# Optimization experiments

Hardware: AMD Instinct MI355X
Metric: run time of the kernel (lower is better)

The kernel has to match this reference:

```python
import jax, jax.numpy as jnp
import numpy as np

H = 64       # hidden_size
V = 200000   # vocab_size
B = 1024     # batch (sessions)
N = 50       # unique nodes per session graph
S = 50       # session sequence length


def setup_inputs() -> dict:
    key = jax.random.key(0)
    ks = jax.random.split(key, 24)
    s = 0.05
    lin = lambda k, i, o: jax.random.normal(k, (i, o), jnp.float32) * s  # stored [in,out]
    return {
        "alias_inputs": jax.random.randint(ks[0], (B, S), 0, N),
        "ain": jax.random.uniform(ks[1], (B, N, N), jnp.float32) * 0.1,
        "aou": jax.random.uniform(ks[2], (B, N, N), jnp.float32) * 0.1,
        "items": jax.random.randint(ks[3], (B, N), 0, V),
        "mask": jnp.ones((B, S), jnp.int32),
        "edge_index": jnp.zeros((2, 1), jnp.int32),
        "emb": jax.random.normal(ks[4], (V, H), jnp.float32) * s,
        "ein_w": lin(ks[5], H, H), "ein_b": jnp.zeros((H,), jnp.float32),
        "eou_w": lin(ks[6], H, H), "eou_b": jnp.zeros((H,), jnp.float32),
        "b_iah": jax.random.normal(ks[7], (H,), jnp.float32) * s,
        "b_oah": jax.random.normal(ks[8], (H,), jnp.float32) * s,
        "igate_w": lin(ks[9], 2 * H, 3 * H), "igate_b": jnp.zeros((3 * H,), jnp.float32),
        "hgate_w": lin(ks[10], H, 3 * H), "hgate_b": jnp.zeros((3 * H,), jnp.float32),
        "fc1_w": lin(ks[11], H, H), "fc1_b": jnp.zeros((H,), jnp.float32),
        "fc2_w": lin(ks[12], H, H), "fc2_b": jnp.zeros((H,), jnp.float32),
        "fc3_w": lin(ks[13], H, 1),
    }


def _forward(alias_inputs, ain, aou, items, mask, emb,
             ein_w, ein_b, eou_w, eou_b, b_iah, b_oah,
             igate_w, igate_b, hgate_w, hgate_b,
             fc1_w, fc1_b, fc2_w, fc2_b, fc3_w):
    STEP = 1
    h = emb[items]  # [B,N,H]
    for _ in range(STEP):
        # GRU-style gated graph conv cell
        input_in = jnp.matmul(ain, h @ ein_w + ein_b) + b_iah    # [B,N,H]
        input_out = jnp.matmul(aou, h @ eou_w + eou_b) + b_oah   # [B,N,H]
        inputs = jnp.concatenate([input_in, input_out], axis=-1)  # [B,N,2H]
        gi = inputs @ igate_w + igate_b                          # [B,N,3H]
        gh = h @ hgate_w + hgate_b                               # [B,N,3H]
        i_r, i_i, i_n = jnp.split(gi, 3, axis=-1)
        h_r, h_i, h_n = jnp.split(gh, 3, axis=-1)
        resetgate = jax.nn.sigmoid(i_r + h_r)
        inputgate = jax.nn.sigmoid(i_i + h_i)
        newgate = jnp.tanh(i_n + resetgate * h_n)
        h = newgate + inputgate * (h - newgate)
    # batch_emb: gather node states back to sequence order
    seq = jnp.take_along_axis(h, alias_inputs[..., None], axis=1)  # [B,S,H]
    # attention readout
    last = jnp.sum(mask, axis=1) - 1                               # [B]
    ht = seq[jnp.arange(seq.shape[0]), last]                       # [B,H]
    q1 = (ht @ fc1_w + fc1_b)[:, None, :]                          # [B,1,H]
    q2 = seq @ fc2_w + fc2_b                                       # [B,S,H]
    alpha = jax.nn.sigmoid(q1 + q2) @ fc3_w                        # [B,S,1]
    a = jnp.sum(alpha * seq * mask[..., None].astype(seq.dtype), axis=1)  # [B,H]
    return a @ emb[1:].T                                           # [B,V-1]


def reference(alias_inputs, ain, aou, items, mask, edge_index, emb,
              ein_w, ein_b, eou_w, eou_b, b_iah, b_oah,
              igate_w, igate_b, hgate_w, hgate_b,
              fc1_w, fc1_b, fc2_w, fc2_b, fc3_w):
    del edge_index  # unused in the original forward
    return _forward(alias_inputs, ain, aou, items, mask, emb,
                    ein_w, ein_b, eou_w, eou_b, b_iah, b_oah,
                    igate_w, igate_b, hgate_w, hgate_b,
                    fc1_w, fc1_b, fc2_w, fc2_b, fc3_w)
```

## Files before the change

kernel.cpp:

```cpp
#include <hip/hip_runtime.h>
#include <math.h>

#define H 64
#define N 50
#define S 50
#define B 1024
#define V 200000
#define VO (V - 1)

__global__ __launch_bounds__(64) void k1_embed_lin(
    const int* __restrict__ items, const float* __restrict__ emb,
    const float* __restrict__ ein_w, const float* __restrict__ ein_b,
    const float* __restrict__ eou_w, const float* __restrict__ eou_b,
    float* __restrict__ h0, float* __restrict__ hv_in, float* __restrict__ hv_out)
{
    int bn = blockIdx.x;
    int j = threadIdx.x;
    __shared__ float hrow[H];
    int item = items[bn];
    float h = emb[(size_t)item * H + j];
    hrow[j] = h;
    h0[(size_t)bn * H + j] = h;
    __syncthreads();
    float si = ein_b[j], so = eou_b[j];
    #pragma unroll
    for (int k = 0; k < H; k++) {
        float x = hrow[k];
        si += x * ein_w[k * H + j];
        so += x * eou_w[k * H + j];
    }
    hv_in[(size_t)bn * H + j] = si;
    hv_out[(size_t)bn * H + j] = so;
}

__global__ __launch_bounds__(64) void k2_adj(
    const float* __restrict__ ain, const float* __restrict__ aou,
    const float* __restrict__ hv_in, const float* __restrict__ hv_out,
    const float* __restrict__ b_iah, const float* __restrict__ b_oah,
    float* __restrict__ in_in, float* __restrict__ in_out)
{
    int bn = blockIdx.x;
    int b = bn / N;
    int j = threadIdx.x;
    const float* ar = ain + (size_t)bn * N;
    const float* br = aou + (size_t)bn * N;
    const float* hin = hv_in + (size_t)b * N * H;
    const float* hou = hv_out + (size_t)b * N * H;
    float si = b_iah[j], so = b_oah[j];
    for (int m = 0; m < N; m++) {
        si += ar[m] * hin[m * H + j];
        so += br[m] * hou[m * H + j];
    }
    in_in[(size_t)bn * H + j] = si;
    in_out[(size_t)bn * H + j] = so;
}

__global__ __launch_bounds__(64) void k3_gru(
    const float* __restrict__ in_in, const float* __restrict__ in_out,
    const float* __restrict__ igate_w, const float* __restrict__ igate_b,
    const float* __restrict__ hgate_w, const float* __restrict__ hgate_b,
    float* __restrict__ h0)
{
    int bn = blockIdx.x;
    int j = threadIdx.x;
    __shared__ float inp[2 * H];
    __shared__ float hrow[H];
    inp[j]     = in_in[(size_t)bn * H + j];
    inp[H + j] = in_out[(size_t)bn * H + j];
    hrow[j]    = h0[(size_t)bn * H + j];
    __syncthreads();
    float gr = igate_b[j], gi = igate_b[H + j], gn = igate_b[2 * H + j];
    for (int k = 0; k < 2 * H; k++) {
        float x = inp[k];
        const float* w = igate_w + (size_t)k * 3 * H;
        gr += x * w[j];
        gi += x * w[H + j];
        gn += x * w[2 * H + j];
    }
    float hr = hgate_b[j], hi = hgate_b[H + j], hn = hgate_b[2 * H + j];
    for (int k = 0; k < H; k++) {
        float x = hrow[k];
        const float* w = hgate_w + (size_t)k * 3 * H;
        hr += x * w[j];
        hi += x * w[H + j];
        hn += x * w[2 * H + j];
    }
    float resetg = 1.f / (1.f + expf(-(gr + hr)));
    float inputg = 1.f / (1.f + expf(-(gi + hi)));
    float newg = tanhf(gn + resetg * hn);
    float h = hrow[j];
    h0[(size_t)bn * H + j] = newg + inputg * (h - newg);
}

__global__ __launch_bounds__(64) void k4_attn(
    const int* __restrict__ alias_in, const int* __restrict__ mask,
    const float* __restrict__ h,
    const float* __restrict__ fc1_w, const float* __restrict__ fc1_b,
    const float* __restrict__ fc2_w, const float* __restrict__ fc2_b,
    const float* __restrict__ fc3_w, float* __restrict__ a)
{
    int b = blockIdx.x;
    int j = threadIdx.x;
    __shared__ float seq[S][H];
    __shared__ float q1s[H];
    const float* hb = h + (size_t)b * N * H;
    for (int s = 0; s < S; s++) {
        int node = alias_in[b * S + s];
        seq[s][j] = hb[(size_t)node * H + j];
    }
    int msum = 0;
    for (int s = 0; s < S; s++) msum += mask[b * S + s];
    int last = msum - 1;
    __syncthreads();
    float q1 = fc1_b[j];
    for (int k = 0; k < H; k++) q1 += seq[last][k] * fc1_w[k * H + j];
    q1s[j] = q1;
    __syncthreads();
    float f3 = fc3_w[j];
    float aj = 0.f;
    for (int s = 0; s < S; s++) {
        float q2 = fc2_b[j];
        for (int k = 0; k < H; k++) q2 += seq[s][k] * fc2_w[k * H + j];
        float v = (1.f / (1.f + expf(-(q1s[j] + q2)))) * f3;
        #pragma unroll
        for (int off = 1; off < 64; off <<= 1) v += __shfl_xor(v, off, 64);
        aj += v * seq[s][j] * (float)mask[b * S + s];
    }
    a[b * H + j] = aj;
}

__global__ __launch_bounds__(256) void k5_out(
    const float* __restrict__ a, const float* __restrict__ emb,
    float* __restrict__ out)
{
    __shared__ __align__(16) float As[64][68];
    __shared__ __align__(16) float Es[64][68];
    int tid = threadIdx.x;
    int tx = tid & 15, ty = tid >> 4;
    int v0 = blockIdx.x * 64;
    int b0 = blockIdx.y * 64;

    for (int idx = tid; idx < 64 * 16; idx += 256) {
        int row = idx >> 4, k4 = idx & 15;
        float4 av = *(const float4*)(a + (size_t)(b0 + row) * H + k4 * 4);
        *(float4*)&As[row][k4 * 4] = av;
        int v = v0 + row;
        float4 ev = make_float4(0.f, 0.f, 0.f, 0.f);
        if (v < VO) ev = *(const float4*)(emb + (size_t)(v + 1) * H + k4 * 4);
        *(float4*)&Es[row][k4 * 4] = ev;
    }
    __syncthreads();

    float acc[4][4] = {};
    #pragma unroll 4
    for (int k4 = 0; k4 < 16; k4++) {
        float4 af[4], ef[4];
        #pragma unroll
        for (int i = 0; i < 4; i++)
            af[i] = *(const float4*)&As[ty + 16 * i][k4 * 4];
        #pragma unroll
        for (int jj = 0; jj < 4; jj++)
            ef[jj] = *(const float4*)&Es[tx + 16 * jj][k4 * 4];
        #pragma unroll
        for (int i = 0; i < 4; i++)
            #pragma unroll
            for (int jj = 0; jj < 4; jj++)
                acc[i][jj] += af[i].x * ef[jj].x + af[i].y * ef[jj].y +
                              af[i].z * ef[jj].z + af[i].w * ef[jj].w;
    }

    #pragma unroll
    for (int i = 0; i < 4; i++) {
        int b = b0 + ty + 16 * i;
        #pragma unroll
        for (int jj = 0; jj < 4; jj++) {
            int v = v0 + tx + 16 * jj;
            if (v < VO) out[(size_t)b * VO + v] = acc[i][jj];
        }
    }
}

extern "C" void kernel_launch(void* const* d_in, const int* in_sizes, int n_in,
                              void* d_out, int out_size, void* d_ws, size_t ws_size,
                              hipStream_t stream)
{
    const int*   alias_in = (const int*)d_in[0];
    const float* ain      = (const float*)d_in[1];
    const float* aou      = (const float*)d_in[2];
    const int*   items    = (const int*)d_in[3];
    const int*   mask     = (const int*)d_in[4];
    const float* emb      = (const float*)d_in[6];
    const float* ein_w    = (const float*)d_in[7];
    const float* ein_b    = (const float*)d_in[8];
    const float* eou_w    = (const float*)d_in[9];
    const float* eou_b    = (const float*)d_in[10];
    const float* b_iah    = (const float*)d_in[11];
    const float* b_oah    = (const float*)d_in[12];
    const float* igate_w  = (const float*)d_in[13];
    const float* igate_b  = (const float*)d_in[14];
    const float* hgate_w  = (const float*)d_in[15];
    const float* hgate_b  = (const float*)d_in[16];
    const float* fc1_w    = (const float*)d_in[17];
    const float* fc1_b    = (const float*)d_in[18];
    const float* fc2_w    = (const float*)d_in[19];
    const float* fc2_b    = (const float*)d_in[20];
    const float* fc3_w    = (const float*)d_in[21];

    float* out = (float*)d_out;

    const size_t NH = (size_t)B * N * H;
    float* h0     = out;
    float* hv_in  = h0 + NH;
    float* hv_out = hv_in + NH;
    float* in_in  = hv_out + NH;
    float* in_out = in_in + NH;
    float* a      = (float*)d_ws;

    k1_embed_lin<<<B * N, 64, 0, stream>>>(items, emb, ein_w, ein_b, eou_w, eou_b,
                                           h0, hv_in, hv_out);
    k2_adj<<<B * N, 64, 0, stream>>>(ain, aou, hv_in, hv_out, b_iah, b_oah,
                                     in_in, in_out);
    k3_gru<<<B * N, 64, 0, stream>>>(in_in, in_out, igate_w, igate_b,
                                     hgate_w, hgate_b, h0);
    k4_attn<<<B, 64, 0, stream>>>(alias_in, mask, h0, fc1_w, fc1_b,
                                  fc2_w, fc2_b, fc3_w, a);
    dim3 g5((VO + 63) / 64, B / 64);
    k5_out<<<g5, 256, 0, stream>>>(a, emb, out);
}
```

Measured before the change: 1.562 ms.

## Retile all kernels with 256-thread blocks and register blocking over rows

Every kernel is restructured. The embedding-linear and GRU kernels now process 32 rows per 256-thread block, with each warp computing 8 rows in registers so weight loads are reused. The adjacency kernel stages a whole session's node features in shared memory once per batch. The attention kernel splits the sequence across 4 warps and caches fc2_w in shared memory. The output GEMM grows to 128x128 tiles with 8x8 per-thread accumulators and an unguarded fast store path. The aim is to cut redundant global weight traffic and raise arithmetic intensity, at the cost of higher register pressure.

```diff
diff --git a/kernel.cpp b/kernel.cpp
--- a/kernel.cpp
+++ b/kernel.cpp
@@ -8,142 +8,247 @@
 #define V 200000
 #define VO (V - 1)
 
-__global__ __launch_bounds__(64) void k1_embed_lin(
+__global__ __launch_bounds__(256) void k1_embed_lin(
     const int* __restrict__ items, const float* __restrict__ emb,
     const float* __restrict__ ein_w, const float* __restrict__ ein_b,
     const float* __restrict__ eou_w, const float* __restrict__ eou_b,
     float* __restrict__ h0, float* __restrict__ hv_in, float* __restrict__ hv_out)
 {
-    int bn = blockIdx.x;
-    int j = threadIdx.x;
-    __shared__ float hrow[H];
-    int item = items[bn];
-    float h = emb[(size_t)item * H + j];
-    hrow[j] = h;
-    h0[(size_t)bn * H + j] = h;
-    __syncthreads();
-    float si = ein_b[j], so = eou_b[j];
+    int tid = threadIdx.x;
+    int j = tid & 63, w = tid >> 6;
+    int bn0 = blockIdx.x * 32;
+    __shared__ __align__(16) float hs[32][H];
+
+    for (int idx = tid; idx < 32 * H; idx += 256) {
+        int row = idx >> 6, col = idx & 63;
+        int item = items[bn0 + row];
+        float hv = emb[(size_t)item * H + col];
+        hs[row][col] = hv;
+        h0[(size_t)(bn0 + row) * H + col] = hv;
+    }
+    __syncthreads();
+
+    float accI[8], accO[8];
+    {
+        float bi = ein_b[j], bo = eou_b[j];
+        #pragma unroll
+        for (int r = 0; r < 8; r++) { accI[r] = bi; accO[r] = bo; }
+    }
+    int base = w * 8;
+    #pragma unroll 4
+    for (int k4 = 0; k4 < 16; k4++) {
+        float4 xv[8];
+        #pragma unroll
+        for (int r = 0; r < 8; r++)
+            xv[r] = *(const float4*)&hs[base + r][k4 * 4];
+        #pragma unroll
+        for (int kk = 0; kk < 4; kk++) {
+            int k = k4 * 4 + kk;
+            float wi = ein_w[k * H + j];
+            float wo = eou_w[k * H + j];
+            #pragma unroll
+            for (int r = 0; r < 8; r++) {
+                float x = ((const float*)&xv[r])[kk];
+                accI[r] += x * wi;
+                accO[r] += x * wo;
+            }
+        }
+    }
     #pragma unroll
-    for (int k = 0; k < H; k++) {
-        float x = hrow[k];
-        si += x * ein_w[k * H + j];
-        so += x * eou_w[k * H + j];
-    }
-    hv_in[(size_t)bn * H + j] = si;
-    hv_out[(size_t)bn * H + j] = so;
-}
-
-__global__ __launch_bounds__(64) void k2_adj(
+    for (int r = 0; r < 8; r++) {
+        hv_in [(size_t)(bn0 + base + r) * H + j] = accI[r];
+        hv_out[(size_t)(bn0 + base + r) * H + j] = accO[r];
+    }
+}
+
+__global__ __launch_bounds__(256) void k2_adj(
     const float* __restrict__ ain, const float* __restrict__ aou,
     const float* __restrict__ hv_in, const float* __restrict__ hv_out,
     const float* __restrict__ b_iah, const float* __restrict__ b_oah,
     float* __restrict__ in_in, float* __restrict__ in_out)
 {
-    int bn = blockIdx.x;
-    int b = bn / N;
-    int j = threadIdx.x;
-    const float* ar = ain + (size_t)bn * N;
-    const float* br = aou + (size_t)bn * N;
-    const float* hin = hv_in + (size_t)b * N * H;
-    const float* hou = hv_out + (size_t)b * N * H;
-    float si = b_iah[j], so = b_oah[j];
-    for (int m = 0; m < N; m++) {
-        si += ar[m] * hin[m * H + j];
-        so += br[m] * hou[m * H + j];
-    }
-    in_in[(size_t)bn * H + j] = si;
-    in_out[(size_t)bn * H + j] = so;
-}
-
-__global__ __launch_bounds__(64) void k3_gru(
+    int tid = threadIdx.x;
+    int j = tid & 63, w = tid >> 6;
+    int b = blockIdx.x;
+    __shared__ float hin_s[N][H];
+    __shared__ float hou_s[N][H];
+
+    for (int idx = tid; idx < N * H; idx += 256) {
+        int row = idx >> 6, col = idx & 63;
+        hin_s[row][col] = hv_in [((size_t)b * N + row) * H + col];
+        hou_s[row][col] = hv_out[((size_t)b * N + row) * H + col];
+    }
+    __syncthreads();
+
+    float bi = b_iah[j], bo = b_oah[j];
+    for (int n = w; n < N; n += 4) {
+        const float* ar = ain + ((size_t)b * N + n) * N;
+        const float* br = aou + ((size_t)b * N + n) * N;
+        float si = bi, so = bo;
+        for (int m = 0; m < N; m++) {
+            si += ar[m] * hin_s[m][j];
+            so += br[m] * hou_s[m][j];
+        }
+        in_in [((size_t)b * N + n) * H + j] = si;
+        in_out[((size_t)b * N + n) * H + j] = so;
+    }
+}
+
+__global__ __launch_bounds__(256) void k3_gru(
     const float* __restrict__ in_in, const float* __restrict__ in_out,
     const float* __restrict__ igate_w, const float* __restrict__ igate_b,
     const float* __restrict__ hgate_w, const float* __restrict__ hgate_b,
     float* __restrict__ h0)
 {
-    int bn = blockIdx.x;
-    int j = threadIdx.x;
-    __shared__ float inp[2 * H];
-    __shared__ float hrow[H];
-    inp[j]     = in_in[(size_t)bn * H + j];
-    inp[H + j] = in_out[(size_t)bn * H + j];
-    hrow[j]    = h0[(size_t)bn * H + j];
-    __syncthreads();
-    float gr = igate_b[j], gi = igate_b[H + j], gn = igate_b[2 * H + j];
-    for (int k = 0; k < 2 * H; k++) {
-        float x = inp[k];
-        const float* w = igate_w + (size_t)k * 3 * H;
-        gr += x * w[j];
-        gi += x * w[H + j];
-        gn += x * w[2 * H + j];
-    }
-    float hr = hgate_b[j], hi = hgate_b[H + j], hn = hgate_b[2 * H + j];
-    for (int k = 0; k < H; k++) {
-        float x = hrow[k];
-        const float* w = hgate_w + (size_t)k * 3 * H;
-        hr += x * w[j];
-        hi += x * w[H + j];
-        hn += x * w[2 * H + j];
-    }
-    float resetg = 1.f / (1.f + expf(-(gr + hr)));
-    float inputg = 1.f / (1.f + expf(-(gi + hi)));
-    float newg = tanhf(gn + resetg * hn);
-    float h = hrow[j];
-    h0[(size_t)bn * H + j] = newg + inputg * (h - newg);
-}
-
-__global__ __launch_bounds__(64) void k4_attn(
+    int tid = threadIdx.x;
+    int j = tid & 63, w = tid >> 6;
+    int bn0 = blockIdx.x * 32;
+    __shared__ __align__(16) float inp_s[32][2 * H];
+    __shared__ __align__(16) float h_s[32][H];
+
+    for (int idx = tid; idx < 32 * H; idx += 256) {
+        int row = idx >> 6, col = idx & 63;
+        size_t g = (size_t)(bn0 + row) * H + col;
+        inp_s[row][col]     = in_in[g];
+        inp_s[row][H + col] = in_out[g];
+        h_s[row][col]       = h0[g];
+    }
+    __syncthreads();
+
+    int base = w * 8;
+    float gr[8], gi[8], gn[8];
+    {
+        float b0v = igate_b[j], b1v = igate_b[H + j], b2v = igate_b[2 * H + j];
+        #pragma unroll
+        for (int r = 0; r < 8; r++) { gr[r] = b0v; gi[r] = b1v; gn[r] = b2v; }
+    }
+    #pragma unroll 2
+    for (int k4 = 0; k4 < 32; k4++) {
+        float4 xv[8];
+        #pragma unroll
+        for (int r = 0; r < 8; r++)
+            xv[r] = *(const float4*)&inp_s[base + r][k4 * 4];
+        #pragma unroll
+        for (int kk = 0; kk < 4; kk++) {
+            int k = k4 * 4 + kk;
+            const float* wrow = igate_w + (size_t)k * 3 * H;
+            float w0 = wrow[j], w1 = wrow[H + j], w2 = wrow[2 * H + j];
+            #pragma unroll
+            for (int r = 0; r < 8; r++) {
+                float x = ((const float*)&xv[r])[kk];
+                gr[r] += x * w0; gi[r] += x * w1; gn[r] += x * w2;
+            }
+        }
+    }
+    float hr[8], hi[8], hn[8];
+    {
+        float b0v = hgate_b[j], b1v = hgate_b[H + j], b2v = hgate_b[2 * H + j];
+        #pragma unroll
+        for (int r = 0; r < 8; r++) { hr[r] = b0v; hi[r] = b1v; hn[r] = b2v; }
+    }
+    #pragma unroll 2
+    for (int k4 = 0; k4 < 16; k4++) {
+        float4 xv[8];
+        #pragma unroll
+        for (int r = 0; r < 8; r++)
+            xv[r] = *(const float4*)&h_s[base + r][k4 * 4];
+        #pragma unroll
+        for (int kk = 0; kk < 4; kk++) {
+            int k = k4 * 4 + kk;
+            const float* wrow = hgate_w + (size_t)k * 3 * H;
+            float w0 = wrow[j], w1 = wrow[H + j], w2 = wrow[2 * H + j];
+            #pragma unroll
+            for (int r = 0; r < 8; r++) {
+                float x = ((const float*)&xv[r])[kk];
+                hr[r] += x * w0; hi[r] += x * w1; hn[r] += x * w2;
+            }
+        }
+    }
+    #pragma unroll
+    for (int r = 0; r < 8; r++) {
+        float resetg = 1.f / (1.f + expf(-(gr[r] + hr[r])));
+        float inputg = 1.f / (1.f + expf(-(gi[r] + hi[r])));
+        float newg = tanhf(gn[r] + resetg * hn[r]);
+        float h = h_s[base + r][j];
+        h0[(size_t)(bn0 + base + r) * H + j] = newg + inputg * (h - newg);
+    }
+}
+
+__global__ __launch_bounds__(256) void k4_attn(
     const int* __restrict__ alias_in, const int* __restrict__ mask,
     const float* __restrict__ h,
     const float* __restrict__ fc1_w, const float* __restrict__ fc1_b,
     const float* __restrict__ fc2_w, const float* __restrict__ fc2_b,
     const float* __restrict__ fc3_w, float* __restrict__ a)
 {
+    int tid = threadIdx.x;
+    int j = tid & 63, w = tid >> 6;
     int b = blockIdx.x;
-    int j = threadIdx.x;
-    __shared__ float seq[S][H];
+    __shared__ __align__(16) float seq_s[S][H];
+    __shared__ float f2s[H][H];
     __shared__ float q1s[H];
-    const float* hb = h + (size_t)b * N * H;
-    for (int s = 0; s < S; s++) {
+    __shared__ float apart[4][H];
+    __shared__ int msum_s;
+
+    for (int idx = tid; idx < S * H; idx += 256) {
+        int s = idx >> 6, c = idx & 63;
         int node = alias_in[b * S + s];
-        seq[s][j] = hb[(size_t)node * H + j];
-    }
-    int msum = 0;
-    for (int s = 0; s < S; s++) msum += mask[b * S + s];
-    int last = msum - 1;
-    __syncthreads();
-    float q1 = fc1_b[j];
-    for (int k = 0; k < H; k++) q1 += seq[last][k] * fc1_w[k * H + j];
-    q1s[j] = q1;
-    __syncthreads();
+        seq_s[s][c] = h[((size_t)b * N + node) * H + c];
+    }
+    for (int idx = tid; idx < H * H; idx += 256)
+        f2s[idx >> 6][idx & 63] = fc2_w[idx];
+    if (tid == 0) {
+        int m = 0;
+        for (int s = 0; s < S; s++) m += mask[b * S + s];
+        msum_s = m;
+    }
+    __syncthreads();
+
+    int last = msum_s - 1;
+    if (w == 0) {
+        float q1 = fc1_b[j];
+        for (int k = 0; k < H; k++) q1 += seq_s[last][k] * fc1_w[k * H + j];
+        q1s[j] = q1;
+    }
+    __syncthreads();
+
     float f3 = fc3_w[j];
+    float q1v = q1s[j];
     float aj = 0.f;
-    for (int s = 0; s < S; s++) {
+    for (int s = w; s < S; s += 4) {
         float q2 = fc2_b[j];
-        for (int k = 0; k < H; k++) q2 += seq[s][k] * fc2_w[k * H + j];
-        float v = (1.f / (1.f + expf(-(q1s[j] + q2)))) * f3;
+        #pragma unroll 4
+        for (int k4 = 0; k4 < 16; k4++) {
+            float4 sv = *(const float4*)&seq_s[s][k4 * 4];
+            q2 += sv.x * f2s[k4 * 4 + 0][j] + sv.y * f2s[k4 * 4 + 1][j]
+                + sv.z * f2s[k4 * 4 + 2][j] + sv.w * f2s[k4 * 4 + 3][j];
+        }
+        float v = (1.f / (1.f + expf(-(q1v + q2)))) * f3;
         #pragma unroll
         for (int off = 1; off < 64; off <<= 1) v += __shfl_xor(v, off, 64);
-        aj += v * seq[s][j] * (float)mask[b * S + s];
-    }
-    a[b * H + j] = aj;
+        aj += v * seq_s[s][j] * (float)mask[b * S + s];
+    }
+    apart[w][j] = aj;
+    __syncthreads();
+    if (w == 0)
+        a[b * H + j] = apart[0][j] + apart[1][j] + apart[2][j] + apart[3][j];
 }
 
 __global__ __launch_bounds__(256) void k5_out(
     const float* __restrict__ a, const float* __restrict__ emb,
     float* __restrict__ out)
 {
-    __shared__ __align__(16) float As[64][68];
-    __shared__ __align__(16) float Es[64][68];
+    __shared__ __align__(16) float As[128][68];
+    __shared__ __align__(16) float Es[128][68];
     int tid = threadIdx.x;
     int tx = tid & 15, ty = tid >> 4;
-    int v0 = blockIdx.x * 64;
-    int b0 = blockIdx.y * 64;
-
-    for (int idx = tid; idx < 64 * 16; idx += 256) {
+    int v0 = blockIdx.x * 128;
+    int b0 = blockIdx.y * 128;
+
+    for (int idx = tid; idx < 128 * 16; idx += 256) {
         int row = idx >> 4, k4 = idx & 15;
-        float4 av = *(const float4*)(a + (size_t)(b0 + row) * H + k4 * 4);
-        *(float4*)&As[row][k4 * 4] = av;
+        *(float4*)&As[row][k4 * 4] =
+            *(const float4*)(a + (size_t)(b0 + row) * H + k4 * 4);
         int v = v0 + row;
         float4 ev = make_float4(0.f, 0.f, 0.f, 0.f);
         if (v < VO) ev = *(const float4*)(emb + (size_t)(v + 1) * H + k4 * 4);
@@ -151,31 +256,41 @@
     }
     __syncthreads();
 
-    float acc[4][4] = {};
-    #pragma unroll 4
+    float acc[8][8] = {};
+    #pragma unroll 2
     for (int k4 = 0; k4 < 16; k4++) {
-        float4 af[4], ef[4];
-        #pragma unroll
-        for (int i = 0; i < 4; i++)
+        float4 af[8], ef[8];
+        #pragma unroll
+        for (int i = 0; i < 8; i++)
             af[i] = *(const float4*)&As[ty + 16 * i][k4 * 4];
         #pragma unroll
-        for (int jj = 0; jj < 4; jj++)
+        for (int jj = 0; jj < 8; jj++)
             ef[jj] = *(const float4*)&Es[tx + 16 * jj][k4 * 4];
         #pragma unroll
-        for (int i = 0; i < 4; i++)
-            #pragma unroll
-            for (int jj = 0; jj < 4; jj++)
+        for (int i = 0; i < 8; i++)
+            #pragma unroll
+            for (int jj = 0; jj < 8; jj++)
                 acc[i][jj] += af[i].x * ef[jj].x + af[i].y * ef[jj].y +
                               af[i].z * ef[jj].z + af[i].w * ef[jj].w;
     }
 
-    #pragma unroll
-    for (int i = 0; i < 4; i++) {
-        int b = b0 + ty + 16 * i;
-        #pragma unroll
-        for (int jj = 0; jj < 4; jj++) {
-            int v = v0 + tx + 16 * jj;
-            if (v < VO) out[(size_t)b * VO + v] = acc[i][jj];
+    if (v0 + 128 <= VO) {
+        #pragma unroll
+        for (int i = 0; i < 8; i++) {
+            size_t bofs = (size_t)(b0 + ty + 16 * i) * VO;
+            #pragma unroll
+            for (int jj = 0; jj < 8; jj++)
+                out[bofs + v0 + tx + 16 * jj] = acc[i][jj];
+        }
+    } else {
+        #pragma unroll
+        for (int i = 0; i < 8; i++) {
+            size_t bofs = (size_t)(b0 + ty + 16 * i) * VO;
+            #pragma unroll
+            for (int jj = 0; jj < 8; jj++) {
+                int v = v0 + tx + 16 * jj;
+                if (v < VO) out[bofs + v] = acc[i][jj];
+            }
         }
     }
 }
@@ -216,14 +331,14 @@
     float* in_out = in_in + NH;
     float* a      = (float*)d_ws;
 
-    k1_embed_lin<<<B * N, 64, 0, stream>>>(items, emb, ein_w, ein_b, eou_w, eou_b,
-                                           h0, hv_in, hv_out);
-    k2_adj<<<B * N, 64, 0, stream>>>(ain, aou, hv_in, hv_out, b_iah, b_oah,
-                                     in_in, in_out);
-    k3_gru<<<B * N, 64, 0, stream>>>(in_in, in_out, igate_w, igate_b,
-                                     hgate_w, hgate_b, h0);
-    k4_attn<<<B, 64, 0, stream>>>(alias_in, mask, h0, fc1_w, fc1_b,
-                                  fc2_w, fc2_b, fc3_w, a);
-    dim3 g5((VO + 63) / 64, B / 64);
+    k1_embed_lin<<<(B * N) / 32, 256, 0, stream>>>(items, emb, ein_w, ein_b,
+                                                   eou_w, eou_b, h0, hv_in, hv_out);
+    k2_adj<<<B, 256, 0, stream>>>(ain, aou, hv_in, hv_out, b_iah, b_oah,
+                                  in_in, in_out);
+    k3_gru<<<(B * N) / 32, 256, 0, stream>>>(in_in, in_out, igate_w, igate_b,
+                                             hgate_w, hgate_b, h0);
+    k4_attn<<<B, 256, 0, stream>>>(alias_in, mask, h0, fc1_w, fc1_b,
+                                   fc2_w, fc2_b, fc3_w, a);
+    dim3 g5((VO + 127) / 128, B / 128);
     k5_out<<<g5, 256, 0, stream>>>(a, emb, out);
 }
```

After: 1.413 ms. -9.5%, faster.
